# Performance work log

Measured on AMD Instinct MI355X. Metric: run time of the kernel, lower is better.

The kernel has to match this reference:

```python
import jax, jax.numpy as jnp
import numpy as np

N, L, N_KNOTS = 512, 64, 9
N_BINS = N_KNOTS - 1
TWO_PI = 2.0 * np.pi


def _circular_conv(x, w, b):
    # x: (N,C,H,W), w: (O,C,3,3); circular (periodic) padding as used for gauge lattices
    xp = jnp.pad(x, ((0, 0), (0, 0), (1, 1), (1, 1)), mode='wrap')
    y = jax.lax.conv_general_dilated(xp, w, (1, 1), 'VALID',
                                     dimension_numbers=('NCHW', 'OIHW', 'NCHW'))
    return y + b[None, :, None, None]


def setup_inputs() -> dict:
    key = jax.random.key(0)
    k1, k2, k3 = jax.random.split(key, 3)
    x = jax.random.normal(k1, (N, L, L), dtype=jnp.float32)
    # partition the lattice into active/passive/frozen masks
    pat = (np.add.outer(np.arange(L), 2 * np.arange(L)) % 3)
    mask_active = jnp.asarray((pat == 0).astype(np.float32))
    mask_passive = jnp.asarray((pat == 1).astype(np.float32))
    mask_frozen = jnp.asarray((pat == 2).astype(np.float32))
    conv1_w = 0.1 * jax.random.normal(k2, (32, 2, 3, 3), dtype=jnp.float32)
    conv1_b = jnp.zeros((32,), jnp.float32)
    conv2_w = 0.1 * jax.random.normal(k3, (3 * N_BINS + 1, 32, 3, 3), dtype=jnp.float32)
    conv2_b = jnp.zeros((3 * N_BINS + 1,), jnp.float32)
    return {"x": x, "mask_active": mask_active, "mask_passive": mask_passive,
            "mask_frozen": mask_frozen, "conv1_w": conv1_w, "conv1_b": conv1_b,
            "conv2_w": conv2_w, "conv2_b": conv2_b}


def reference(x, mask_active, mask_passive, mask_frozen, conv1_w, conv1_b, conv2_w, conv2_b):
    nb = N_BINS
    # prepare_u1_input: frozen-masked (cos, sin) channels
    net_in = mask_frozen[None, None] * jnp.stack([jnp.cos(x), jnp.sin(x)], axis=1)  # (N,2,L,L)
    h1 = jax.nn.gelu(_circular_conv(net_in, conv1_w, conv1_b))
    net_out = _circular_conv(h1, conv2_w, conv2_b)              # (N,3nb+1,L,L)
    net_out = jnp.transpose(net_out, (0, 2, 3, 1))              # (N,L,L,3nb+1)
    w = jax.nn.softmax(net_out[..., :nb], axis=-1)
    h = jax.nn.softmax(net_out[..., nb:2 * nb], axis=-1)
    d = jax.nn.softplus(net_out[..., 2 * nb:3 * nb])
    t = net_out[..., -1]
    # circular knots on [0, 2pi]; periodic derivative: s[-1] = s[0]
    zeros = jnp.zeros(w.shape[:-1] + (1,), w.dtype)
    kx = jnp.concatenate([zeros, TWO_PI * jnp.cumsum(w, -1)], -1)   # (N,L,L,n_knots)
    ky = jnp.concatenate([zeros, TWO_PI * jnp.cumsum(h, -1)], -1)
    s = jnp.concatenate([d, d[..., :1]], -1)
    # dir = 0 (forward): x1 = active * mod(x)
    x1 = mask_active[None] * jnp.remainder(x, TWO_PI)
    # bin search over interior knots -> k in [0, nb-1]
    k = jnp.sum((x1[..., None] >= kx[..., 1:-1]).astype(jnp.int32), axis=-1)
    g = lambda a, i: jnp.take_along_axis(a, i[..., None], axis=-1)[..., 0]
    kxk, kxk1 = g(kx, k), g(kx, k + 1)
    kyk, kyk1 = g(ky, k), g(ky, k + 1)
    sk, sk1 = g(s, k), g(s, k + 1)
    wk = kxk1 - kxk
    hk = kyk1 - kyk
    slope = hk / wk
    xi = jnp.clip((x1 - kxk) / wk, 0.0, 1.0)
    om = 1.0 - xi
    # rational-quadratic spline (Durkan et al. 2019)
    den = slope + (sk1 + sk - 2.0 * slope) * xi * om
    y = kyk + hk * (slope * xi * xi + sk * xi * om) / den
    local_logJ = jnp.log(slope * slope * (sk1 * xi * xi + 2.0 * slope * xi * om + sk * om * om)) \
                 - 2.0 * jnp.log(den)
    fx1 = mask_active[None] * (y + t)              # (1-dir)*t with dir=0
    local_logJ = mask_active[None] * local_logJ
    logJ = jnp.sum(local_logJ, axis=(1, 2))
    fx = mask_active[None] * jnp.remainder(fx1, TWO_PI) + mask_passive[None] * x + mask_frozen[None] * x
    return fx, logJ
```

## Files before the change

kernel.cpp:

```cpp
#include <hip/hip_runtime.h>
#include <math.h>

#define Nn 512
#define Ld 64
#define NB 8
#define C1 32
#define C2 25

__device__ __forceinline__ float gelu_tanh(float a) {
    float a3 = a * a * a;
    float t = tanhf(0.7978845608028654f * (a + 0.044715f * a3));
    return 0.5f * a * (1.0f + t);
}

__device__ __forceinline__ float softplus_f(float v) {
    return (v > 0.0f) ? v + log1pf(expf(-v)) : log1pf(expf(v));
}

__device__ __forceinline__ float pos_mod_2pi(float v) {
    const float T = 6.2831853071795864769f;
    float r = fmodf(v, T);
    if (r < 0.0f) r += T;
    return r;
}

__global__ __launch_bounds__(256, 8) void k1_conv1_kernel(
    const float* __restrict__ x,
    const float* __restrict__ c1w, const float* __restrict__ c1b,
    float* __restrict__ h1g)
{
    __shared__ float s_cos[8 * 69];
    __shared__ float s_sin[8 * 69];

    const int tid = threadIdx.x;
    const int rb  = blockIdx.x;
    const int n   = blockIdx.y;
    const int r0k = rb * 4;
    const float* xn = x + n * 4096;

    for (int idx = tid; idx < 8 * 68; idx += 256) {
        int li = idx / 68, lj = idx - li * 68;
        int gi = (r0k - 2 + li) & 63;
        int gj = (lj - 2) & 63;
        float xv = xn[gi * 64 + gj];
        int pat = (gi + 2 * gj) % 3;
        float sv, cv;
        sincosf(xv, &sv, &cv);
        float fz = (pat == 2) ? 1.0f : 0.0f;
        s_cos[li * 69 + lj] = fz * cv;
        s_sin[li * 69 + lj] = fz * sv;
    }
    __syncthreads();

    const int gj = tid & 63, lrow = tid >> 6;
    const int gi = r0k + lrow;

    float v[18];
    #pragma unroll
    for (int di = 0; di < 3; ++di)
        #pragma unroll
        for (int dj = 0; dj < 3; ++dj) {
            int a = (lrow + 1 + di) * 69 + (gj + 1 + dj);
            v[di * 3 + dj]     = s_cos[a];
            v[9 + di * 3 + dj] = s_sin[a];
        }

    float* outp = h1g + (size_t)n * C1 * 4096 + gi * 64 + gj;
    #pragma unroll 4
    for (int c = 0; c < C1; ++c) {
        const float* w = c1w + c * 18;
        float a1 = c1b[c];
        #pragma unroll
        for (int t = 0; t < 9; ++t) {
            a1 = fmaf(v[t],     w[t],     a1);
            a1 = fmaf(v[9 + t], w[9 + t], a1);
        }
        outp[(size_t)c * 4096] = gelu_tanh(a1);
    }
}

#define K2CH 4
#define K2PLANE (14 * 64)

__global__ __launch_bounds__(256, 8) void k2_conv2_spline_kernel(
    const float* __restrict__ x, const float* __restrict__ h1g,
    const float* __restrict__ c2w, const float* __restrict__ c2b,
    float* __restrict__ out_fx, float* __restrict__ out_logJ)
{
    __shared__ float s_h1[K2CH * K2PLANE];
    __shared__ float s_red[4];

    const float TWO_PI_F = 6.2831853071795864769f;

    const int tid  = threadIdx.x;
    const int band = blockIdx.x;
    const int n    = blockIdx.y;
    const int r0   = band * 12;
    const int R    = (band == 5) ? 4 : 12;
    const int rows_l   = R + 2;
    const int n_active = (R == 12) ? 256 : 86;
    const float* xn  = x + n * 4096;
    const float* h1n = h1g + (size_t)n * C1 * 4096;

    int g3 = tid >> 6, u = tid & 63;
    int rsel  = (u >= 22) + (u >= 43);
    int ubase = (rsel == 2) ? 43 : ((rsel == 1) ? 22 : 0);
    int rr = 3 * g3 + rsel;
    int cc = 3 * (u - ubase) + rsel;
    bool is_act = (tid < n_active);
    int jm = (cc + 63) & 63, jp = (cc + 1) & 63;

    float acc[C2];
    #pragma unroll
    for (int co = 0; co < C2; ++co) acc[co] = c2b[co];

    for (int c0 = 0; c0 < C1; c0 += K2CH) {
        __syncthreads();
        int nf4 = K2CH * rows_l * 16;
        for (int f = tid; f < nf4; f += 256) {
            int c   = f / (rows_l * 16);
            int rem = f - c * (rows_l * 16);
            int r = rem >> 4, cg = rem & 15;
            int grow = (r0 - 1 + r) & 63;
            float4 src = *(const float4*)(h1n + (size_t)(c0 + c) * 4096 + grow * 64 + cg * 4);
            *(float4*)(&s_h1[c * K2PLANE + r * 64 + cg * 4]) = src;
        }
        __syncthreads();
        if (is_act) {
            #pragma unroll 1
            for (int c = 0; c < K2CH; ++c) {
                int ci = c0 + c;
                float v[9];
                #pragma unroll
                for (int di = 0; di < 3; ++di) {
                    const float* rowp = s_h1 + c * K2PLANE + (rr + di) * 64;
                    v[di * 3 + 0] = rowp[jm];
                    v[di * 3 + 1] = rowp[cc];
                    v[di * 3 + 2] = rowp[jp];
                }
                const float* wp = c2w + ci * 9;
                #pragma unroll
                for (int co = 0; co < C2; ++co) {
                    const float* w = wp + co * (C1 * 9);
                    float a2 = acc[co];
                    #pragma unroll
                    for (int t = 0; t < 9; ++t) a2 = fmaf(v[t], w[t], a2);
                    acc[co] = a2;
                }
            }
        }
    }

    float* outn = out_fx + n * 4096;
    for (int idx = tid; idx < R * 64; idx += 256) {
        int lr = idx >> 6, c = idx & 63;
        int gi = r0 + lr;
        int pat = (gi + 2 * c) % 3;
        float xv = xn[gi * 64 + c];
        if (pat != 0) outn[gi * 64 + c] = xv;
    }

    float lj_val = 0.0f;
    if (is_act) {
        int gi = r0 + rr;
        float xv = xn[gi * 64 + cc];

        float kx[NB + 1], ky[NB + 1], sar[NB + 1];
        {
            float m = acc[0];
            #pragma unroll
            for (int q = 1; q < NB; ++q) m = fmaxf(m, acc[q]);
            float e[NB], ssum = 0.0f;
            #pragma unroll
            for (int q = 0; q < NB; ++q) { e[q] = expf(acc[q] - m); ssum += e[q]; }
            float inv = TWO_PI_F / ssum;
            float run = 0.0f;
            kx[0] = 0.0f;
            #pragma unroll
            for (int q = 0; q < NB; ++q) { run += e[q]; kx[q + 1] = run * inv; }
        }
        {
            float m = acc[NB];
            #pragma unroll
            for (int q = 1; q < NB; ++q) m = fmaxf(m, acc[NB + q]);
            float e[NB], ssum = 0.0f;
            #pragma unroll
            for (int q = 0; q < NB; ++q) { e[q] = expf(acc[NB + q] - m); ssum += e[q]; }
            float inv = TWO_PI_F / ssum;
            float run = 0.0f;
            ky[0] = 0.0f;
            #pragma unroll
            for (int q = 0; q < NB; ++q) { run += e[q]; ky[q + 1] = run * inv; }
        }
        #pragma unroll
        for (int q = 0; q < NB; ++q) sar[q] = softplus_f(acc[2 * NB + q]);
        sar[NB] = sar[0];
        float t_out = acc[3 * NB];

        float x1 = pos_mod_2pi(xv);
        int k = 0;
        #pragma unroll
        for (int q = 1; q <= NB - 1; ++q) k += (x1 >= kx[q]) ? 1 : 0;

        float kxk = 0.f, kxk1 = 0.f, kyk = 0.f, kyk1 = 0.f, sk = 0.f, sk1 = 0.f;
        #pragma unroll
        for (int q = 0; q <= NB; ++q) {
            if (q == k)     { kxk = kx[q];  kyk = ky[q];  sk  = sar[q]; }
            if (q == k + 1) { kxk1 = kx[q]; kyk1 = ky[q]; sk1 = sar[q]; }
        }

        float wk = kxk1 - kxk;
        float hk = kyk1 - kyk;
        float slope = hk / wk;
        float xi = (x1 - kxk) / wk;
        xi = fminf(fmaxf(xi, 0.0f), 1.0f);
        float om = 1.0f - xi;
        float den = slope + (sk1 + sk - 2.0f * slope) * xi * om;
        float y = kyk + hk * (slope * xi * xi + sk * xi * om) / den;
        float num = slope * slope * (sk1 * xi * xi + 2.0f * slope * xi * om + sk * om * om);
        lj_val = logf(num) - 2.0f * logf(den);

        outn[gi * 64 + cc] = pos_mod_2pi(y + t_out);
    }

    float r = lj_val;
    #pragma unroll
    for (int off = 32; off > 0; off >>= 1) r += __shfl_down(r, off, 64);
    int lane = tid & 63, wv = tid >> 6;
    if (lane == 0) s_red[wv] = r;
    __syncthreads();
    if (tid == 0)
        atomicAdd(&out_logJ[n], s_red[0] + s_red[1] + s_red[2] + s_red[3]);
}

#define CHUNK 8
#define ICOLS 68
#define ISTR  69
#define IROWSMAX 16
#define HCOLS 66
#define HSTR  67
#define HPLANE 945

__global__ __launch_bounds__(256, 4) void csplaq_v4_kernel(
    const float* __restrict__ x,
    const float* __restrict__ c1w, const float* __restrict__ c1b,
    const float* __restrict__ c2w, const float* __restrict__ c2b,
    float* __restrict__ out_fx, float* __restrict__ out_logJ)
{
    __shared__ float s_cos[IROWSMAX * ISTR];
    __shared__ float s_sin[IROWSMAX * ISTR];
    __shared__ float s_h1[CHUNK * HPLANE];
    __shared__ float s_red[4];

    const float TWO_PI_F = 6.2831853071795864769f;
    const int tid  = threadIdx.x;
    const int band = blockIdx.x;
    const int n    = blockIdx.y;
    const int r0   = band * 12;
    const int R    = (band == 5) ? 4 : 12;
    const int rows_in  = R + 4;
    const int nsite_h  = (R + 2) * HCOLS;
    const int n_active = (R == 12) ? 256 : 86;
    const float* xn = x + n * Ld * Ld;

    for (int idx = tid; idx < rows_in * ICOLS; idx += 256) {
        int li = idx / ICOLS, uu = idx - li * ICOLS;
        int gi = (r0 - 2 + li) & 63;
        int gj = (uu - 2) & 63;
        float xv = xn[gi * Ld + gj];
        int pat = (gi + 2 * gj) % 3;
        float sv, cv;
        sincosf(xv, &sv, &cv);
        float fz = (pat == 2) ? 1.0f : 0.0f;
        s_cos[li * ISTR + uu] = fz * cv;
        s_sin[li * ISTR + uu] = fz * sv;
    }

    int g3 = tid >> 6, u = tid & 63;
    int rsel  = (u >= 22) + (u >= 43);
    int ubase = (rsel == 2) ? 43 : ((rsel == 1) ? 22 : 0);
    int rr = 3 * g3 + rsel;
    int cc = 3 * (u - ubase) + rsel;
    bool is_act = (tid < n_active);

    float acc[C2];
    #pragma unroll
    for (int co = 0; co < C2; ++co) acc[co] = c2b[co];

    for (int c0 = 0; c0 < C1; c0 += CHUNK) {
        __syncthreads();
        for (int s = tid; s < nsite_h; s += 256) {
            int h = s / HCOLS, j = s - h * HCOLS;
            float v[18];
            #pragma unroll
            for (int di = 0; di < 3; ++di)
                #pragma unroll
                for (int dj = 0; dj < 3; ++dj) {
                    int a = (h + di) * ISTR + (j + dj);
                    v[di * 3 + dj]     = s_cos[a];
                    v[9 + di * 3 + dj] = s_sin[a];
                }
            #pragma unroll
            for (int c = 0; c < CHUNK; ++c) {
                const float* w = c1w + (c0 + c) * 18;
                float a1 = c1b[c0 + c];
                #pragma unroll
                for (int t = 0; t < 9; ++t) {
                    a1 = fmaf(v[t],     w[t],     a1);
                    a1 = fmaf(v[9 + t], w[9 + t], a1);
                }
                s_h1[c * HPLANE + h * HSTR + j] = gelu_tanh(a1);
            }
        }
        __syncthreads();
        if (is_act) {
            #pragma unroll 1
            for (int c = 0; c < CHUNK; ++c) {
                int ci = c0 + c;
                float v[9];
                const float* hp = s_h1 + c * HPLANE + rr * HSTR + cc;
                #pragma unroll
                for (int di = 0; di < 3; ++di)
                    #pragma unroll
                    for (int dj = 0; dj < 3; ++dj)
                        v[di * 3 + dj] = hp[di * HSTR + dj];
                const float* wp = c2w + ci * 9;
                #pragma unroll
                for (int co = 0; co < C2; ++co) {
                    const float* w = wp + co * (C1 * 9);
                    float a2 = acc[co];
                    #pragma unroll
                    for (int t = 0; t < 9; ++t) a2 = fmaf(v[t], w[t], a2);
                    acc[co] = a2;
                }
            }
        }
    }

    float* outn = out_fx + n * Ld * Ld;
    for (int idx = tid; idx < R * 64; idx += 256) {
        int lr = idx >> 6, c = idx & 63;
        int gi = r0 + lr;
        int pat = (gi + 2 * c) % 3;
        float xv = xn[gi * Ld + c];
        if (pat != 0) outn[gi * Ld + c] = xv;
    }

    float lj_val = 0.0f;
    if (is_act) {
        int gi = r0 + rr;
        float xv = xn[gi * Ld + cc];
        float kx[NB + 1], ky[NB + 1], sar[NB + 1];
        {
            float m = acc[0];
            #pragma unroll
            for (int q = 1; q < NB; ++q) m = fmaxf(m, acc[q]);
            float e[NB], ssum = 0.0f;
            #pragma unroll
            for (int q = 0; q < NB; ++q) { e[q] = expf(acc[q] - m); ssum += e[q]; }
            float inv = TWO_PI_F / ssum;
            float run = 0.0f;
            kx[0] = 0.0f;
            #pragma unroll
            for (int q = 0; q < NB; ++q) { run += e[q]; kx[q + 1] = run * inv; }
        }
        {
            float m = acc[NB];
            #pragma unroll
            for (int q = 1; q < NB; ++q) m = fmaxf(m, acc[NB + q]);
            float e[NB], ssum = 0.0f;
            #pragma unroll
            for (int q = 0; q < NB; ++q) { e[q] = expf(acc[NB + q] - m); ssum += e[q]; }
            float inv = TWO_PI_F / ssum;
            float run = 0.0f;
            ky[0] = 0.0f;
            #pragma unroll
            for (int q = 0; q < NB; ++q) { run += e[q]; ky[q + 1] = run * inv; }
        }
        #pragma unroll
        for (int q = 0; q < NB; ++q) sar[q] = softplus_f(acc[2 * NB + q]);
        sar[NB] = sar[0];
        float t_out = acc[3 * NB];

        float x1 = pos_mod_2pi(xv);
        int k = 0;
        #pragma unroll
        for (int q = 1; q <= NB - 1; ++q) k += (x1 >= kx[q]) ? 1 : 0;

        float kxk = 0.f, kxk1 = 0.f, kyk = 0.f, kyk1 = 0.f, sk = 0.f, sk1 = 0.f;
        #pragma unroll
        for (int q = 0; q <= NB; ++q) {
            if (q == k)     { kxk = kx[q];  kyk = ky[q];  sk  = sar[q]; }
            if (q == k + 1) { kxk1 = kx[q]; kyk1 = ky[q]; sk1 = sar[q]; }
        }

        float wk = kxk1 - kxk;
        float hk = kyk1 - kyk;
        float slope = hk / wk;
        float xi = (x1 - kxk) / wk;
        xi = fminf(fmaxf(xi, 0.0f), 1.0f);
        float om = 1.0f - xi;
        float den = slope + (sk1 + sk - 2.0f * slope) * xi * om;
        float y = kyk + hk * (slope * xi * xi + sk * xi * om) / den;
        float num = slope * slope * (sk1 * xi * xi + 2.0f * slope * xi * om + sk * om * om);
        lj_val = logf(num) - 2.0f * logf(den);

        outn[gi * Ld + cc] = pos_mod_2pi(y + t_out);
    }

    float r = lj_val;
    #pragma unroll
    for (int off = 32; off > 0; off >>= 1) r += __shfl_down(r, off, 64);
    int lane = tid & 63, wv = tid >> 6;
    if (lane == 0) s_red[wv] = r;
    __syncthreads();
    if (tid == 0)
        atomicAdd(&out_logJ[n], s_red[0] + s_red[1] + s_red[2] + s_red[3]);
}

extern "C" void kernel_launch(void* const* d_in, const int* in_sizes, int n_in,
                              void* d_out, int out_size, void* d_ws, size_t ws_size,
                              hipStream_t stream) {
    const float* x   = (const float*)d_in[0];
    const float* c1w = (const float*)d_in[4];
    const float* c1b = (const float*)d_in[5];
    const float* c2w = (const float*)d_in[6];
    const float* c2b = (const float*)d_in[7];

    float* out_fx   = (float*)d_out;
    float* out_logJ = out_fx + (size_t)Nn * Ld * Ld;

    hipMemsetAsync(out_logJ, 0, Nn * sizeof(float), stream);

    const size_t h1_bytes = (size_t)Nn * C1 * Ld * Ld * sizeof(float);
    if (ws_size >= h1_bytes) {
        float* h1g = (float*)d_ws;
        dim3 g1(16, Nn);
        k1_conv1_kernel<<<g1, 256, 0, stream>>>(x, c1w, c1b, h1g);
        dim3 g2(6, Nn);
        k2_conv2_spline_kernel<<<g2, 256, 0, stream>>>(x, h1g, c2w, c2b, out_fx, out_logJ);
    } else {
        dim3 grid(6, Nn);
        csplaq_v4_kernel<<<grid, 256, 0, stream>>>(x, c1w, c1b, c2w, c2b, out_fx, out_logJ);
    }
}
```

Before: 396.7 us.

## Store conv1 activations channel-last and read them directly in conv2 without LDS

Conv1 now writes its hidden activations in a pixel-major, channel-minor layout, using float4 stores of four channels at a time. Conv2 drops the shared-memory staging loop and its barriers. Each active thread instead gathers its 3x3 neighbourhood straight from global memory, four channels per float4 load. This removes LDS traffic and synchronisation but relies on L1/L2 to serve overlapping neighbour reads. The 32-channel pixel stride makes adjacent threads' loads strided rather than coalesced, and the launch bounds are relaxed.

```diff
diff --git a/kernel.cpp b/kernel.cpp
--- a/kernel.cpp
+++ b/kernel.cpp
@@ -24,7 +24,7 @@
     return r;
 }
 
-__global__ __launch_bounds__(256, 8) void k1_conv1_kernel(
+__global__ __launch_bounds__(256) void k1_conv1_cm_kernel(
     const float* __restrict__ x,
     const float* __restrict__ c1w, const float* __restrict__ c1b,
     float* __restrict__ h1g)
@@ -65,29 +65,32 @@
             v[9 + di * 3 + dj] = s_sin[a];
         }
 
-    float* outp = h1g + (size_t)n * C1 * 4096 + gi * 64 + gj;
-    #pragma unroll 4
-    for (int c = 0; c < C1; ++c) {
-        const float* w = c1w + c * 18;
-        float a1 = c1b[c];
-        #pragma unroll
-        for (int t = 0; t < 9; ++t) {
-            a1 = fmaf(v[t],     w[t],     a1);
-            a1 = fmaf(v[9 + t], w[9 + t], a1);
-        }
-        outp[(size_t)c * 4096] = gelu_tanh(a1);
-    }
-}
-
-#define K2CH 4
-#define K2PLANE (14 * 64)
-
-__global__ __launch_bounds__(256, 8) void k2_conv2_spline_kernel(
+    float* h1p = h1g + ((size_t)n * 4096 + gi * 64 + gj) * 32;
+    #pragma unroll 2
+    for (int cg = 0; cg < 8; ++cg) {
+        float oo[4];
+        #pragma unroll
+        for (int cs = 0; cs < 4; ++cs) {
+            int c = cg * 4 + cs;
+            const float* w = c1w + c * 18;
+            float a1 = c1b[c];
+            #pragma unroll
+            for (int t = 0; t < 9; ++t) {
+                a1 = fmaf(v[t],     w[t],     a1);
+                a1 = fmaf(v[9 + t], w[9 + t], a1);
+            }
+            oo[cs] = gelu_tanh(a1);
+        }
+        float4 o; o.x = oo[0]; o.y = oo[1]; o.z = oo[2]; o.w = oo[3];
+        *(float4*)(h1p + cg * 4) = o;
+    }
+}
+
+__global__ __launch_bounds__(256, 4) void k2_conv2_spline_cm_kernel(
     const float* __restrict__ x, const float* __restrict__ h1g,
     const float* __restrict__ c2w, const float* __restrict__ c2b,
     float* __restrict__ out_fx, float* __restrict__ out_logJ)
 {
-    __shared__ float s_h1[K2CH * K2PLANE];
     __shared__ float s_red[4];
 
     const float TWO_PI_F = 6.2831853071795864769f;
@@ -97,10 +100,9 @@
     const int n    = blockIdx.y;
     const int r0   = band * 12;
     const int R    = (band == 5) ? 4 : 12;
-    const int rows_l   = R + 2;
     const int n_active = (R == 12) ? 256 : 86;
     const float* xn  = x + n * 4096;
-    const float* h1n = h1g + (size_t)n * C1 * 4096;
+    const float* h1n = h1g + (size_t)n * 4096 * 32;
 
     int g3 = tid >> 6, u = tid & 63;
     int rsel  = (u >= 22) + (u >= 43);
@@ -114,37 +116,32 @@
     #pragma unroll
     for (int co = 0; co < C2; ++co) acc[co] = c2b[co];
 
-    for (int c0 = 0; c0 < C1; c0 += K2CH) {
-        __syncthreads();
-        int nf4 = K2CH * rows_l * 16;
-        for (int f = tid; f < nf4; f += 256) {
-            int c   = f / (rows_l * 16);
-            int rem = f - c * (rows_l * 16);
-            int r = rem >> 4, cg = rem & 15;
-            int grow = (r0 - 1 + r) & 63;
-            float4 src = *(const float4*)(h1n + (size_t)(c0 + c) * 4096 + grow * 64 + cg * 4);
-            *(float4*)(&s_h1[c * K2PLANE + r * 64 + cg * 4]) = src;
-        }
-        __syncthreads();
-        if (is_act) {
-            #pragma unroll 1
-            for (int c = 0; c < K2CH; ++c) {
-                int ci = c0 + c;
-                float v[9];
-                #pragma unroll
-                for (int di = 0; di < 3; ++di) {
-                    const float* rowp = s_h1 + c * K2PLANE + (rr + di) * 64;
-                    v[di * 3 + 0] = rowp[jm];
-                    v[di * 3 + 1] = rowp[cc];
-                    v[di * 3 + 2] = rowp[jp];
-                }
-                const float* wp = c2w + ci * 9;
+    if (is_act) {
+        int gi = r0 + rr;
+        int rows[3] = { (gi + 63) & 63, gi, (gi + 1) & 63 };
+        int cols[3] = { jm, cc, jp };
+        const float* p[9];
+        #pragma unroll
+        for (int di = 0; di < 3; ++di)
+            #pragma unroll
+            for (int dj = 0; dj < 3; ++dj)
+                p[di * 3 + dj] = h1n + ((size_t)(rows[di] * 64 + cols[dj])) * 32;
+
+        #pragma unroll 1
+        for (int cb = 0; cb < 8; ++cb) {
+            float arr[36];
+            #pragma unroll
+            for (int t = 0; t < 9; ++t)
+                *(float4*)(&arr[t * 4]) = *(const float4*)(p[t] + cb * 4);
+            #pragma unroll
+            for (int cs = 0; cs < 4; ++cs) {
+                const float* wp = c2w + (cb * 4 + cs) * 9;
                 #pragma unroll
                 for (int co = 0; co < C2; ++co) {
                     const float* w = wp + co * (C1 * 9);
                     float a2 = acc[co];
                     #pragma unroll
-                    for (int t = 0; t < 9; ++t) a2 = fmaf(v[t], w[t], a2);
+                    for (int t = 0; t < 9; ++t) a2 = fmaf(arr[t * 4 + cs], w[t], a2);
                     acc[co] = a2;
                 }
             }
@@ -436,9 +433,9 @@
     if (ws_size >= h1_bytes) {
         float* h1g = (float*)d_ws;
         dim3 g1(16, Nn);
-        k1_conv1_kernel<<<g1, 256, 0, stream>>>(x, c1w, c1b, h1g);
+        k1_conv1_cm_kernel<<<g1, 256, 0, stream>>>(x, c1w, c1b, h1g);
         dim3 g2(6, Nn);
-        k2_conv2_spline_kernel<<<g2, 256, 0, stream>>>(x, h1g, c2w, c2b, out_fx, out_logJ);
+        k2_conv2_spline_cm_kernel<<<g2, 256, 0, stream>>>(x, h1g, c2w, c2b, out_fx, out_logJ);
     } else {
         dim3 grid(6, Nn);
         csplaq_v4_kernel<<<grid, 256, 0, stream>>>(x, c1w, c1b, c2w, c2b, out_fx, out_logJ);
```

After: 728.9 us. 1.84x slower.
